# Performance work log

Hardware: AMD Instinct MI355X
Metric: run time of the kernel (lower is better)

## Reference

```python
import jax, jax.numpy as jnp
import numpy as np

# BlendParams defaults (pytorch3d)
SIGMA = 1e-4
GAMMA = 1e-4
BG_BLUE = 1.0       # background_color = (1,1,1); module returns channel 2
ZNEAR = 1.0
ZFAR = 100.0
EPS = 1e-10

N, H, W, K = 8, 256, 256, 50


def setup_inputs() -> dict:
    key = jax.random.key(0)
    k1, k2, k3 = jax.random.split(key, 3)
    # depth buffer values in [znear, zfar]
    zbuf = jax.random.uniform(k1, (N, H, W, K), dtype=jnp.float32) * (ZFAR - ZNEAR) + ZNEAR
    # signed (squared) pixel-to-edge distances: small magnitudes near 0
    dists = jax.random.normal(k2, (N, H, W, K), dtype=jnp.float32) * 1e-3
    # face indices; -1 marks empty slots (~1/100000 here, plus explicit tail masking)
    pix_to_face = jax.random.randint(k3, (N, H, W, K), -1, 100000, dtype=jnp.int64)
    # make the last few K-slots empty, as a real rasterizer would
    slot = jnp.arange(K)
    pix_to_face = jnp.where(slot < K - 5, pix_to_face, jnp.int64(-1))
    return {"zbuf": zbuf, "dists": dists, "pix_to_face": pix_to_face}


def reference(zbuf, dists, pix_to_face):
    # softmax_rgb_blend with colors == zbuf broadcast over 3 channels;
    # the module returns images[..., 2] (blue channel of the blended RGBA).
    mask = (pix_to_face >= 0).astype(zbuf.dtype)                      # (N,H,W,K)
    prob = jax.nn.sigmoid(-dists / SIGMA) * mask                      # distance sigmoid
    # z-based softmax weights (stabilized by per-pixel max)
    z_inv = (ZFAR - zbuf) / (ZFAR - ZNEAR) * mask                     # (N,H,W,K)
    z_inv_max = jnp.maximum(jnp.max(z_inv, axis=-1, keepdims=True), EPS)
    weights_num = prob * jnp.exp((z_inv - z_inv_max) / GAMMA)         # (N,H,W,K)
    delta = jnp.maximum(jnp.exp((EPS - z_inv_max) / GAMMA), EPS)      # (N,H,W,1)
    denom = jnp.sum(weights_num, axis=-1, keepdims=True) + delta      # (N,H,W,1)
    # weighted color sum; all three channels equal zbuf, take channel 2
    weighted = jnp.sum(weights_num * zbuf, axis=-1, keepdims=True)    # (N,H,W,1)
    blue = (weighted + delta * BG_BLUE) / denom                       # (N,H,W,1)
    return blue[..., 0]                                               # (N,H,W)
```

## Files before the change

### kernel.cpp

```cpp
#include <hip/hip_runtime.h>


constexpr int THREADS = 512;
constexpr int WAVES   = THREADS / 64;
constexpr int TILE_PX = 128;
constexpr int PX_B    = 200;
constexpr int ARR_B   = TILE_PX * PX_B;
constexpr int BUF_B   = 3 * ARR_B;
constexpr int ASTEPS  = ARR_B / 1024;
constexpr int STEPS   = 3 * ASTEPS;
constexpr int NBLOCKS = 256;

constexpr float INV_SIGMA  = 1e4f;
constexpr float INVG       = 1e4f;
constexpr float ZFAR       = 100.0f;
constexpr float ZRANGE     = 99.0f;
constexpr float INV_ZRANGE = 1.0f / 99.0f;
constexpr float EPS        = 1e-10f;

#define GLDS16(gp, lp) __builtin_amdgcn_global_load_lds(                     \
    (const __attribute__((address_space(1))) void*)(gp),                     \
    (__attribute__((address_space(3))) void*)(lp), 16, 0, 0)

__device__ __forceinline__ void pixel_blend(
    const int2 fa, const int2 fb, const int2 fc, const int2 fd,
    const float2 za, const float2 zb, const float2 zc, const float2 zd,
    const float2 da, const float2 db, const float2 dc, const float2 dd,
    const bool tail_owner,
    float& m_out, float& s1_out, float& s2_out)
{
    const bool m0 = (fa.x >= 0),               m1 = (fa.y >= 0);
    const bool m2 = (fb.x >= 0),               m3 = (fb.y >= 0);
    const bool m4 = (fc.x >= 0),               m5 = (fc.y >= 0);
    const bool m6 = tail_owner && (fd.x >= 0), m7 = tail_owner && (fd.y >= 0);

    float zv[8], pv[8];
    zv[0] = m0 ? (ZFAR - za.x) * INV_ZRANGE : 0.0f;
    zv[1] = m1 ? (ZFAR - za.y) * INV_ZRANGE : 0.0f;
    zv[2] = m2 ? (ZFAR - zb.x) * INV_ZRANGE : 0.0f;
    zv[3] = m3 ? (ZFAR - zb.y) * INV_ZRANGE : 0.0f;
    zv[4] = m4 ? (ZFAR - zc.x) * INV_ZRANGE : 0.0f;
    zv[5] = m5 ? (ZFAR - zc.y) * INV_ZRANGE : 0.0f;
    zv[6] = m6 ? (ZFAR - zd.x) * INV_ZRANGE : 0.0f;
    zv[7] = m7 ? (ZFAR - zd.y) * INV_ZRANGE : 0.0f;
    pv[0] = m0 ? 1.0f / (1.0f + __expf(da.x * INV_SIGMA)) : 0.0f;
    pv[1] = m1 ? 1.0f / (1.0f + __expf(da.y * INV_SIGMA)) : 0.0f;
    pv[2] = m2 ? 1.0f / (1.0f + __expf(db.x * INV_SIGMA)) : 0.0f;
    pv[3] = m3 ? 1.0f / (1.0f + __expf(db.y * INV_SIGMA)) : 0.0f;
    pv[4] = m4 ? 1.0f / (1.0f + __expf(dc.x * INV_SIGMA)) : 0.0f;
    pv[5] = m5 ? 1.0f / (1.0f + __expf(dc.y * INV_SIGMA)) : 0.0f;
    pv[6] = m6 ? 1.0f / (1.0f + __expf(dd.x * INV_SIGMA)) : 0.0f;
    pv[7] = m7 ? 1.0f / (1.0f + __expf(dd.y * INV_SIGMA)) : 0.0f;

    float m = fmaxf(fmaxf(fmaxf(zv[0], zv[1]), fmaxf(zv[2], zv[3])),
                    fmaxf(fmaxf(zv[4], zv[5]), fmaxf(zv[6], zv[7])));
    m = fmaxf(m, __shfl_xor(m, 1));
    m = fmaxf(m, __shfl_xor(m, 2));
    m = fmaxf(m, __shfl_xor(m, 4));
    m = fmaxf(m, EPS);

    float S1a = 0.0f, S1b = 0.0f, S2a = 0.0f, S2b = 0.0f;
    #pragma unroll
    for (int j = 0; j < 8; j += 2) {
        const float w0 = pv[j]   * __expf((zv[j]   - m) * INVG);
        const float w1 = pv[j+1] * __expf((zv[j+1] - m) * INVG);
        S1a += w0;
        S1b += w1;
        S2a += w0 * (ZFAR - zv[j]   * ZRANGE);
        S2b += w1 * (ZFAR - zv[j+1] * ZRANGE);
    }
    float S1 = S1a + S1b;
    float S2 = S2a + S2b;
    S1 += __shfl_xor(S1, 1);  S1 += __shfl_xor(S1, 2);  S1 += __shfl_xor(S1, 4);
    S2 += __shfl_xor(S2, 1);  S2 += __shfl_xor(S2, 2);  S2 += __shfl_xor(S2, 4);

    m_out = m;  s1_out = S1;  s2_out = S2;
}

__global__ __launch_bounds__(THREADS, 1) void soft_depth_kernel(
    const float* __restrict__ zbuf,
    const float* __restrict__ dists,
    const int*   __restrict__ p2f,
    float*       __restrict__ out,
    const int tiles_per_block)
{
    __shared__ __align__(16) char smem[2 * BUF_B];

    const int t    = threadIdx.x;
    const int lane = t & 63;
    const int wid  = t >> 6;
    const int q    = t & 7;
    const int team = t >> 3;

    const char* __restrict__ zc = (const char*)zbuf;
    const char* __restrict__ dc = (const char*)dists;
    const char* __restrict__ fc = (const char*)p2f;

    const int tile0 = blockIdx.x * tiles_per_block;

    auto stage = [&](int tile, char* buf) {
        const size_t tb = (size_t)tile * ARR_B;
        const char* zt = zc + tb;
        const char* dt = dc + tb;
        const char* ft = fc + tb;
        for (int s = wid; s < STEPS; s += WAVES) {
            const int a = s / ASTEPS;
            const int j = s - a * ASTEPS;
            const char* g = (a == 0) ? zt : (a == 1) ? dt : ft;
            GLDS16(g + j * 1024 + lane * 16, buf + a * ARR_B + j * 1024);
        }
    };

    auto compute = [&](int tile, const char* buf) {
        const float2* __restrict__ zl = (const float2*)(buf);
        const float2* __restrict__ dl = (const float2*)(buf + ARR_B);
        const int2*   __restrict__ fl = (const int2*)(buf + 2 * ARR_B);

        const int pA  = 2 * team;
        const int cbA = pA * 25;
        const int cbB = cbA + 25;
        const int a0 = cbA + q, a1 = cbA + q + 8, a2 = cbA + q + 16, a3 = cbA + 24;
        const int b0 = cbB + q, b1 = cbB + q + 8, b2 = cbB + q + 16, b3 = cbB + 24;

        const int2   fA0 = fl[a0], fA1 = fl[a1], fA2 = fl[a2], fA3 = fl[a3];
        const int2   fB0 = fl[b0], fB1 = fl[b1], fB2 = fl[b2], fB3 = fl[b3];
        const float2 zA0 = zl[a0], zA1 = zl[a1], zA2 = zl[a2], zA3 = zl[a3];
        const float2 zB0 = zl[b0], zB1 = zl[b1], zB2 = zl[b2], zB3 = zl[b3];
        const float2 dA0 = dl[a0], dA1 = dl[a1], dA2 = dl[a2], dA3 = dl[a3];
        const float2 dB0 = dl[b0], dB1 = dl[b1], dB2 = dl[b2], dB3 = dl[b3];

        const bool town = (q == 0);
        float mA, S1A, S2A, mB, S1B, S2B;
        pixel_blend(fA0, fA1, fA2, fA3, zA0, zA1, zA2, zA3,
                    dA0, dA1, dA2, dA3, town, mA, S1A, S2A);
        pixel_blend(fB0, fB1, fB2, fB3, zB0, zB1, zB2, zB3,
                    dB0, dB1, dB2, dB3, town, mB, S1B, S2B);

        if (q < 2) {
            const float m  = (q == 0) ? mA  : mB;
            const float s1 = (q == 0) ? S1A : S1B;
            const float s2 = (q == 0) ? S2A : S2B;
            const float delta = fmaxf(__expf((EPS - m) * INVG), EPS);
            out[(size_t)tile * TILE_PX + pA + q] = (s2 + delta) / (s1 + delta);
        }
    };

    int cur = 0;
    stage(tile0, smem);
    asm volatile("s_waitcnt vmcnt(0)" ::: "memory");
    __builtin_amdgcn_s_barrier();
    __builtin_amdgcn_sched_barrier(0);

    for (int i = 0; i < tiles_per_block; ++i) {
        if (i + 1 < tiles_per_block)
            stage(tile0 + i + 1, smem + (cur ^ 1) * BUF_B);
        __builtin_amdgcn_sched_barrier(0);
        compute(tile0 + i, smem + cur * BUF_B);
        asm volatile("s_waitcnt vmcnt(0)" ::: "memory");
        __builtin_amdgcn_s_barrier();
        __builtin_amdgcn_sched_barrier(0);
        cur ^= 1;
    }
}

extern "C" void kernel_launch(void* const* d_in, const int* in_sizes, int n_in,
                              void* d_out, int out_size, void* d_ws, size_t ws_size,
                              hipStream_t stream) {
    const float* zbuf  = (const float*)d_in[0];
    const float* dists = (const float*)d_in[1];
    const int*   p2f   = (const int*)d_in[2];
    float* out = (float*)d_out;

    const int pixels = out_size;
    const int tiles  = pixels / TILE_PX;
    const int tpb    = tiles / NBLOCKS;

    soft_depth_kernel<<<dim3(NBLOCKS), dim3(THREADS), 0, stream>>>(
        zbuf, dists, p2f, out, tpb);
}
```

Measured before the change: 298.6 us.

## Use partial vmcnt waits and more blocks for finer-grained LDS double buffering

Replaces the full vmcnt(0) wait after each compute with per-wave partial waits before compute, so only the current tile's loads must land while the next tile's loads stay in flight. The grid becomes 256 blocks of 16 tiles each (pixels/2048), and launch bounds allow 2 blocks per CU, though the 150KB LDS footprint likely still limits residency. Divides switch to __fdividef. The hand-counted vmcnt values depend on the exact per-wave load count and are fragile if the compiler reorders or adds memory ops.

Result: no change. 299.1 us (+0.2%).

```diff
diff --git a/kernel.cpp b/kernel.cpp
--- a/kernel.cpp
+++ b/kernel.cpp
@@ -1,15 +1,14 @@
 #include <hip/hip_runtime.h>
 
 
-constexpr int THREADS = 512;
-constexpr int WAVES   = THREADS / 64;
-constexpr int TILE_PX = 128;
-constexpr int PX_B    = 200;
-constexpr int ARR_B   = TILE_PX * PX_B;
-constexpr int BUF_B   = 3 * ARR_B;
-constexpr int ASTEPS  = ARR_B / 1024;
-constexpr int STEPS   = 3 * ASTEPS;
-constexpr int NBLOCKS = 256;
+constexpr int THREADS  = 512;
+constexpr int WAVES    = THREADS / 64;
+constexpr int TILE_PX  = 128;
+constexpr int PX_B     = 200;
+constexpr int ARR_B    = TILE_PX * PX_B;
+constexpr int BUF_B    = 3 * ARR_B;
+constexpr int STEPS    = BUF_B / 1024;
+constexpr int TILES_PB = 16;
 
 constexpr float INV_SIGMA  = 1e4f;
 constexpr float INVG       = 1e4f;
@@ -21,6 +20,8 @@
 #define GLDS16(gp, lp) __builtin_amdgcn_global_load_lds(                     \
     (const __attribute__((address_space(1))) void*)(gp),                     \
     (__attribute__((address_space(3))) void*)(lp), 16, 0, 0)
+
+#define VMWAIT(N) asm volatile("s_waitcnt vmcnt(" #N ")" ::: "memory")
 
 __device__ __forceinline__ void pixel_blend(
     const int2 fa, const int2 fb, const int2 fc, const int2 fd,
@@ -43,14 +44,14 @@
     zv[5] = m5 ? (ZFAR - zc.y) * INV_ZRANGE : 0.0f;
     zv[6] = m6 ? (ZFAR - zd.x) * INV_ZRANGE : 0.0f;
     zv[7] = m7 ? (ZFAR - zd.y) * INV_ZRANGE : 0.0f;
-    pv[0] = m0 ? 1.0f / (1.0f + __expf(da.x * INV_SIGMA)) : 0.0f;
-    pv[1] = m1 ? 1.0f / (1.0f + __expf(da.y * INV_SIGMA)) : 0.0f;
-    pv[2] = m2 ? 1.0f / (1.0f + __expf(db.x * INV_SIGMA)) : 0.0f;
-    pv[3] = m3 ? 1.0f / (1.0f + __expf(db.y * INV_SIGMA)) : 0.0f;
-    pv[4] = m4 ? 1.0f / (1.0f + __expf(dc.x * INV_SIGMA)) : 0.0f;
-    pv[5] = m5 ? 1.0f / (1.0f + __expf(dc.y * INV_SIGMA)) : 0.0f;
-    pv[6] = m6 ? 1.0f / (1.0f + __expf(dd.x * INV_SIGMA)) : 0.0f;
-    pv[7] = m7 ? 1.0f / (1.0f + __expf(dd.y * INV_SIGMA)) : 0.0f;
+    pv[0] = m0 ? __fdividef(1.0f, 1.0f + __expf(da.x * INV_SIGMA)) : 0.0f;
+    pv[1] = m1 ? __fdividef(1.0f, 1.0f + __expf(da.y * INV_SIGMA)) : 0.0f;
+    pv[2] = m2 ? __fdividef(1.0f, 1.0f + __expf(db.x * INV_SIGMA)) : 0.0f;
+    pv[3] = m3 ? __fdividef(1.0f, 1.0f + __expf(db.y * INV_SIGMA)) : 0.0f;
+    pv[4] = m4 ? __fdividef(1.0f, 1.0f + __expf(dc.x * INV_SIGMA)) : 0.0f;
+    pv[5] = m5 ? __fdividef(1.0f, 1.0f + __expf(dc.y * INV_SIGMA)) : 0.0f;
+    pv[6] = m6 ? __fdividef(1.0f, 1.0f + __expf(dd.x * INV_SIGMA)) : 0.0f;
+    pv[7] = m7 ? __fdividef(1.0f, 1.0f + __expf(dd.y * INV_SIGMA)) : 0.0f;
 
     float m = fmaxf(fmaxf(fmaxf(zv[0], zv[1]), fmaxf(zv[2], zv[3])),
                     fmaxf(fmaxf(zv[4], zv[5]), fmaxf(zv[6], zv[7])));
@@ -77,12 +78,11 @@
     m_out = m;  s1_out = S1;  s2_out = S2;
 }
 
-__global__ __launch_bounds__(THREADS, 1) void soft_depth_kernel(
+__global__ __launch_bounds__(THREADS, 2) void soft_depth_kernel(
     const float* __restrict__ zbuf,
     const float* __restrict__ dists,
     const int*   __restrict__ p2f,
-    float*       __restrict__ out,
-    const int tiles_per_block)
+    float*       __restrict__ out)
 {
     __shared__ __align__(16) char smem[2 * BUF_B];
 
@@ -96,17 +96,16 @@
     const char* __restrict__ dc = (const char*)dists;
     const char* __restrict__ fc = (const char*)p2f;
 
-    const int tile0 = blockIdx.x * tiles_per_block;
+    const int tile0 = blockIdx.x * TILES_PB;
+    const bool nw10 = (wid < 3);
 
     auto stage = [&](int tile, char* buf) {
         const size_t tb = (size_t)tile * ARR_B;
-        const char* zt = zc + tb;
-        const char* dt = dc + tb;
-        const char* ft = fc + tb;
+        #pragma unroll 1
         for (int s = wid; s < STEPS; s += WAVES) {
-            const int a = s / ASTEPS;
-            const int j = s - a * ASTEPS;
-            const char* g = (a == 0) ? zt : (a == 1) ? dt : ft;
+            const int a = s / 25;
+            const int j = s - a * 25;
+            const char* g = (a == 0) ? zc + tb : (a == 1) ? dc + tb : fc + tb;
             GLDS16(g + j * 1024 + lane * 16, buf + a * ARR_B + j * 1024);
         }
     };
@@ -141,25 +140,31 @@
             const float s1 = (q == 0) ? S1A : S1B;
             const float s2 = (q == 0) ? S2A : S2B;
             const float delta = fmaxf(__expf((EPS - m) * INVG), EPS);
-            out[(size_t)tile * TILE_PX + pA + q] = (s2 + delta) / (s1 + delta);
+            out[(size_t)tile * TILE_PX + pA + q] =
+                __fdividef(s2 + delta, s1 + delta);
         }
     };
 
-    int cur = 0;
     stage(tile0, smem);
-    asm volatile("s_waitcnt vmcnt(0)" ::: "memory");
-    __builtin_amdgcn_s_barrier();
-    __builtin_amdgcn_sched_barrier(0);
 
-    for (int i = 0; i < tiles_per_block; ++i) {
-        if (i + 1 < tiles_per_block)
-            stage(tile0 + i + 1, smem + (cur ^ 1) * BUF_B);
+    #pragma unroll 1
+    for (int i = 0; i < TILES_PB; ++i) {
+        const char* cbuf = smem + (i & 1) * BUF_B;
+        if (i + 1 < TILES_PB)
+            stage(tile0 + i + 1, smem + ((i + 1) & 1) * BUF_B);
+
+        if (i == 0)                { if (nw10) VMWAIT(10); else VMWAIT(9);  }
+        else if (i + 1 < TILES_PB) { if (nw10) VMWAIT(11); else VMWAIT(10); }
+        else                       { VMWAIT(1); }
         __builtin_amdgcn_sched_barrier(0);
-        compute(tile0 + i, smem + cur * BUF_B);
-        asm volatile("s_waitcnt vmcnt(0)" ::: "memory");
         __builtin_amdgcn_s_barrier();
         __builtin_amdgcn_sched_barrier(0);
-        cur ^= 1;
+
+        compute(tile0 + i, cbuf);
+
+        __builtin_amdgcn_sched_barrier(0);
+        __builtin_amdgcn_s_barrier();
+        __builtin_amdgcn_sched_barrier(0);
     }
 }
 
@@ -172,9 +177,8 @@
     float* out = (float*)d_out;
 
     const int pixels = out_size;
-    const int tiles  = pixels / TILE_PX;
-    const int tpb    = tiles / NBLOCKS;
+    const int blocks = pixels / (TILE_PX * TILES_PB);
 
-    soft_depth_kernel<<<dim3(NBLOCKS), dim3(THREADS), 0, stream>>>(
-        zbuf, dists, p2f, out, tpb);
+    soft_depth_kernel<<<dim3(blocks), dim3(THREADS), 0, stream>>>(
+        zbuf, dists, p2f, out);
 }
```
